# Kernel tuning notes

Hardware: AMD Instinct MI355X
Metric: run time of the kernel (lower is better)

Reference implementation:

```python
import jax, jax.numpy as jnp
import numpy as np

B, L, E = 64, 512, 512       # batch, encoder length, encoder dim
T = 512                      # decoder steps
S, P = 512, 256              # symbols_embedding_dim, prenet_dim
A, D = 1024, 1024            # attention_rnn_dim, decoder_rnn_dim
G, V = 128, 148              # gmm hidden, n_symbols


def setup_inputs() -> dict:
    key = jax.random.key(0)
    ks = jax.random.split(key, 20)
    w = lambda k, shp, s=0.02: (jax.random.normal(k, shp, dtype=jnp.float32) * s)
    memory = jax.random.normal(ks[0], (B, L, E), dtype=jnp.float32)
    decoder_inputs = jax.random.normal(ks[1], (B, S, T), dtype=jnp.float32)
    memory_lengths = jax.random.randint(ks[2], (B,), L // 2, L + 1)
    memory_lengths = memory_lengths.at[0].set(L)  # max length == L (static shapes)
    return {
        'memory': memory,
        'decoder_inputs': decoder_inputs,
        'memory_lengths': memory_lengths,
        'W_pre1': w(ks[3], (S, P)), 'W_pre2': w(ks[4], (P, P)),
        'W_att_ih': w(ks[5], (P + E, 4 * A)), 'W_att_hh': w(ks[6], (A, 4 * A)),
        'b_att_ih': jnp.zeros((4 * A,), jnp.float32), 'b_att_hh': jnp.zeros((4 * A,), jnp.float32),
        'W_g1': w(ks[7], (A, G)), 'b_g1': jnp.zeros((G,), jnp.float32),
        'W_g2': w(ks[8], (G, 2), 0.01),  # original inits this to zero; small random to exercise math
        'W_dec_ih': w(ks[9], (A + E, 4 * D)), 'W_dec_hh': w(ks[10], (D, 4 * D)),
        'b_dec_ih': jnp.zeros((4 * D,), jnp.float32), 'b_dec_hh': jnp.zeros((4 * D,), jnp.float32),
        'W_proj': w(ks[11], (D + E, V)), 'b_proj': jnp.zeros((V,), jnp.float32),
    }


def _lstm_cell(x, h, c, Wih, Whh, bih, bhh):
    # torch.nn.LSTMCell gate order: i, f, g, o
    g = x @ Wih + h @ Whh + bih + bhh
    i, f, gg, o = jnp.split(g, 4, axis=-1)
    c = jax.nn.sigmoid(f) * c + jax.nn.sigmoid(i) * jnp.tanh(gg)
    h = jax.nn.sigmoid(o) * jnp.tanh(c)
    return h, c


def _forward(memory, decoder_inputs, memory_lengths,
             W_pre1, W_pre2, W_att_ih, W_att_hh, b_att_ih, b_att_hh,
             W_g1, b_g1, W_g2, W_dec_ih, W_dec_hh, b_dec_ih, b_dec_hh,
             W_proj, b_proj):
    Bv, Sv, Tv = decoder_inputs.shape
    Lv = memory.shape[1]
    # go frame + teacher-forced inputs: (T+1, B, S)
    x = jnp.concatenate([jnp.zeros((1, Bv, Sv), memory.dtype),
                         jnp.transpose(decoder_inputs, (2, 0, 1))], axis=0)
    # Prenet: dropout is hardcoded training=True in the original
    dk1, dk2 = jax.random.split(jax.random.key(42))
    h1 = jax.nn.relu(x @ W_pre1)
    h1 = h1 * jax.random.bernoulli(dk1, 0.5, h1.shape).astype(h1.dtype) * 2.0
    h2 = jax.nn.relu(h1 @ W_pre2)
    pre = h2 * jax.random.bernoulli(dk2, 0.5, h2.shape).astype(h2.dtype) * 2.0  # (T+1,B,P)

    pad_mask = jnp.arange(Lv)[None, :] >= memory_lengths[:, None]  # (B,L) True on padding
    lin = jnp.arange(Lv, dtype=memory.dtype)[None, :]              # (1,L)

    Av, Dv, Ev = W_att_hh.shape[0], W_dec_hh.shape[0], memory.shape[2]
    init = (jnp.zeros((Bv, Av), memory.dtype), jnp.zeros((Bv, Av), memory.dtype),
            jnp.zeros((Bv, Dv), memory.dtype), jnp.zeros((Bv, Dv), memory.dtype),
            jnp.zeros((Bv, Lv), memory.dtype),  # cumulative attention weights
            jnp.zeros((Bv, Ev), memory.dtype),  # attention context
            jnp.zeros((Bv, 1), memory.dtype))   # GMM mean mu

    def step(carry, x_t):
        ah, ac, dh, dc, cum, ctx, mean = carry
        ah, ac = _lstm_cell(jnp.concatenate([x_t, ctx], -1), ah, ac,
                            W_att_ih, W_att_hh, b_att_ih, b_att_hh)
        # (eval mode: p_attention_dropout inactive)
        h = jnp.tanh(ah @ W_g1 + b_g1) @ W_g2          # (B,2) raw [mean_delta, scale]
        mean = mean + jnp.exp(h[:, :1]) * 8.0
        scale = jnp.exp(h[:, 1:]) * 8.0
        Z = jnp.sqrt(2.0 * np.pi * scale * scale)
        alpha = jnp.exp(-0.5 * (lin - mean) ** 2 / (scale * scale)) / Z  # (B,L)
        alpha = jnp.where(pad_mask, 0.0, alpha)
        ctx = jnp.einsum('bl,ble->be', alpha, memory)
        cum = cum + alpha
        dh, dc = _lstm_cell(jnp.concatenate([ah, ctx], -1), dh, dc,
                            W_dec_ih, W_dec_hh, b_dec_ih, b_dec_hh)
        logit = jnp.concatenate([dh, ctx], -1) @ W_proj + b_proj
        return (ah, ac, dh, dc, cum, ctx, mean), (logit, alpha, h)

    _, (logits, aligns, params) = jax.lax.scan(step, init, pre[:-1])
    return (jnp.transpose(logits, (1, 0, 2)),   # (B,T,V)
            jnp.transpose(aligns, (1, 0, 2)),   # (B,T,L)
            jnp.transpose(params, (1, 0, 2)))   # (B,T,2)


def reference(memory, decoder_inputs, memory_lengths, W_pre1, W_pre2,
              W_att_ih, W_att_hh, b_att_ih, b_att_hh, W_g1, b_g1, W_g2,
              W_dec_ih, W_dec_hh, b_dec_ih, b_dec_hh, W_proj, b_proj):
    return _forward(memory, decoder_inputs, memory_lengths, W_pre1, W_pre2,
                    W_att_ih, W_att_hh, b_att_ih, b_att_hh, W_g1, b_g1, W_g2,
                    W_dec_ih, W_dec_hh, b_dec_ih, b_dec_hh, W_proj, b_proj)
```

## Files before the change

kernel.cpp:

```cpp
#include <hip/hip_runtime.h>
#include <math.h>

#define TF_PARTITIONABLE 1

static constexpr int Bn=64, Ln=512, En=512, Tn=512, Sn=512, Pn=256, An=1024, Dn=1024, Gn=128, Vn=148;
static constexpr int G4A = 4096;
static constexpr int KPROJ = Dn + En;
static constexpr int KATT = 1792, KDEC = 2560;
static constexpr int ACH = 4, ACK = 448;
static constexpr int DCH = 4, DCK = 640;
static constexpr int NKB_ATT = KATT / 32;
static constexpr int NKB_DEC = KDEC / 32;
static constexpr long LOGITS_OFF = 0;
static constexpr long ALIGNS_OFF = (long)Bn*Tn*Vn;
static constexpr long PARAMS_OFF = ALIGNS_OFF + (long)Bn*Tn*Ln;

using s16x8 = __attribute__((ext_vector_type(8))) short;
using f32x4 = __attribute__((ext_vector_type(4))) float;

struct TFo { unsigned a, b; };
static constexpr TFo htf(unsigned k1, unsigned k2, unsigned x0, unsigned x1) {
  unsigned ks2 = k1 ^ k2 ^ 0x1BD11BDAu;
  unsigned ks[3] = {k1, k2, ks2};
  const unsigned ra[4] = {13u,15u,26u,6u}, rb[4] = {17u,29u,16u,24u};
  x0 += k1; x1 += k2;
  for (int g = 0; g < 5; ++g) {
    const unsigned* r = (g % 2 == 0) ? ra : rb;
    for (int i = 0; i < 4; ++i) { x0 += x1; x1 = (x1 << r[i]) | (x1 >> (32u - r[i])); x1 ^= x0; }
    x0 += ks[(g+1)%3]; x1 += ks[(g+2)%3] + (unsigned)(g+1);
  }
  return TFo{x0, x1};
}
#if TF_PARTITIONABLE
static constexpr TFo DK1 = htf(0u,42u,0u,0u);
static constexpr TFo DK2 = htf(0u,42u,0u,1u);
#else
static constexpr TFo S02 = htf(0u,42u,0u,2u);
static constexpr TFo S13 = htf(0u,42u,1u,3u);
static constexpr TFo DK1 = TFo{S02.a, S13.a};
static constexpr TFo DK2 = TFo{S02.b, S13.b};
#endif

__device__ __forceinline__ void dtf(unsigned k1, unsigned k2, unsigned x0, unsigned x1,
                                    unsigned& o0, unsigned& o1) {
  unsigned ks2 = k1 ^ k2 ^ 0x1BD11BDAu;
#define TFR(r) { x0 += x1; x1 = (x1<<r)|(x1>>(32-r)); x1 ^= x0; }
  x0 += k1; x1 += k2;
  TFR(13) TFR(15) TFR(26) TFR(6)  x0 += k2;  x1 += ks2 + 1u;
  TFR(17) TFR(29) TFR(16) TFR(24) x0 += ks2; x1 += k1 + 2u;
  TFR(13) TFR(15) TFR(26) TFR(6)  x0 += k1;  x1 += k2 + 3u;
  TFR(17) TFR(29) TFR(16) TFR(24) x0 += k2;  x1 += ks2 + 4u;
  TFR(13) TFR(15) TFR(26) TFR(6)  x0 += ks2; x1 += k1 + 5u;
#undef TFR
  o0 = x0; o1 = x1;
}

__device__ __forceinline__ bool keepmask(unsigned ka, unsigned kb, unsigned j) {
#if TF_PARTITIONABLE
  unsigned o0, o1; dtf(ka, kb, 0u, j, o0, o1);
  return ((o0 ^ o1) >> 31) == 0u;
#else
  const unsigned H = 4202496u;
  unsigned o0, o1;
  if (j < H) { dtf(ka, kb, j, j + H, o0, o1); return (o0 >> 31) == 0u; }
  else       { dtf(ka, kb, j - H, j, o0, o1); return (o1 >> 31) == 0u; }
#endif
}

__device__ __forceinline__ float ldbf(const unsigned short* p, long i) {
  return __uint_as_float(((unsigned)p[i]) << 16);
}
__device__ __forceinline__ unsigned short f2bf(float v) {
  unsigned x = __float_as_uint(v);
  return (unsigned short)((x + 0x7fffu + ((x >> 16) & 1u)) >> 16);
}
__device__ __forceinline__ void store_out(void* out, long i, float v, int bf) {
  if (bf) ((unsigned short*)out)[i] = f2bf(v);
  else    ((float*)out)[i] = v;
}
__device__ __forceinline__ float st_load(const float* p, long i) { return p[i]; }
__device__ __forceinline__ float st_load(const unsigned short* p, long i) { return ldbf(p, i); }
__device__ __forceinline__ void st_store(float* p, long i, float v) { p[i] = v; }
__device__ __forceinline__ void st_store(unsigned short* p, long i, float v) { p[i] = f2bf(v); }
__device__ __forceinline__ float sigm(float x) { return 1.f / (1.f + expf(-x)); }
__device__ __forceinline__ void st4bf(unsigned short* p, float a, float b, float c, float d) {
  union { unsigned short u[4]; uint2 v; } q;
  q.u[0] = f2bf(a); q.u[1] = f2bf(b); q.u[2] = f2bf(c); q.u[3] = f2bf(d);
  *(uint2*)p = q.v;
}

struct Ptrs {
  const float *Wp1,*Wp2,*bai,*bah,*Wg1,*bg1,*Wg2,*bdi,*bdh,*Wpr,*bpr;
  unsigned short *PWatt,*PWdec,*pre_bf,*ah_bf,*ctx_bf,*dh_bf;
  float *Patt,*Pdec,*ac,*dc,*mean;
  void *dh_all,*ctx_all;
  const void *mem,*din,*w_ai,*w_ah,*w_di,*w_dh;
  const int *mlen; const int *flag; void *out;
};

__global__ __launch_bounds__(256) void k_detect(const void* mem, int* flag) {
  __shared__ int cnt;
  int tid = threadIdx.x;
  if (tid == 0) cnt = 0;
  __syncthreads();
  const unsigned short* p = (const unsigned short*)mem;
  int local = 0;
  for (int i = tid; i < 1024; i += 256) {
    float f = ldbf(p, 2L * i);
    if (f == f && fabsf(f) > 0.0009f && fabsf(f) < 16.f) local++;
  }
  atomicAdd(&cnt, local);
  __syncthreads();
  if (tid == 0) flag[0] = (cnt > 512) ? 1 : 0;
}

__global__ __launch_bounds__(256) void k_convert(const void* src, float* dst, long n, const int* flag) {
  int bf = *flag;
  long i0 = (long)blockIdx.x * 256 + threadIdx.x, stp = (long)gridDim.x * 256;
  if (bf) { const unsigned short* s = (const unsigned short*)src;
            for (long i = i0; i < n; i += stp) dst[i] = ldbf(s, i); }
  else    { const float* s = (const float*)src;
            for (long i = i0; i < n; i += stp) dst[i] = s[i]; }
}

__global__ __launch_bounds__(256) void k_zero_f32(float* p, long n) {
  for (long i = (long)blockIdx.x * 256 + threadIdx.x; i < n; i += (long)gridDim.x * 256) p[i] = 0.f;
}

__global__ __launch_bounds__(256) void k_zero_aligns(void* out, const int* flag) {
  int bf = *flag;
  unsigned* p; long n;
  if (bf) { p = (unsigned*)out + (ALIGNS_OFF >> 1); n = ((long)Bn*Tn*Ln) >> 1; }
  else    { p = (unsigned*)out + ALIGNS_OFF;        n = (long)Bn*Tn*Ln; }
  for (long i = (long)blockIdx.x * 256 + threadIdx.x; i < n; i += (long)gridDim.x * 256) p[i] = 0u;
}

__global__ __launch_bounds__(256) void k_pack(Ptrs P) {
  __shared__ float s[32][65];
  int bid = blockIdx.x, tid = threadIdx.x;
  bool att = bid < NKB_ATT * 64;
  int lb = att ? bid : bid - NKB_ATT * 64;
  int kblk = lb >> 6, ng = lb & 63;
  int n0 = ng * 64;
  int bf = *P.flag;
  int split = att ? (Pn + En) : (An + En);
  const void* S0 = att ? P.w_ai : P.w_di;
  const void* S1 = att ? P.w_ah : P.w_dh;
  for (int i = tid; i < 2048; i += 256) {
    int kk = i >> 6, n = i & 63;
    int k = kblk * 32 + kk;
    const void* src = (k < split) ? S0 : S1;
    long idx = (long)(k < split ? k : k - split) * G4A + (n0 + n);
    s[kk][n] = bf ? ldbf((const unsigned short*)src, idx) : ((const float*)src)[idx];
  }
  __syncthreads();
  int lane = tid & 63, tb = tid >> 6;
  unsigned short r[8];
#pragma unroll
  for (int j = 0; j < 8; ++j)
    r[j] = f2bf(s[(lane >> 4) * 8 + j][tb * 16 + (lane & 15)]);
  unsigned short* out = (att ? P.PWatt : P.PWdec) +
      (((long)kblk * 256 + (ng * 4 + tb)) * 64 + lane) * 8;
  *(uint4*)out = *(const uint4*)r;
}

__global__ __launch_bounds__(256) void k_prenet(Ptrs P, unsigned k1a, unsigned k1b,
                                                unsigned k2a, unsigned k2b) {
  __shared__ __align__(16) float x_s[32 * 17];
  __shared__ __align__(16) float W_s[16 * 256];
  __shared__ __align__(16) float h1_s[32 * 258];
  int bid = blockIdx.x, tid = threadIdx.x;
  int t = bid >> 1, half = bid & 1;
  int bf = *P.flag;
  int tc = tid & 63, tr = tid >> 6;
  int p0 = tc * 4, bl0 = tr * 8;
  float acc[8][4];
#pragma unroll
  for (int i = 0; i < 8; ++i) { acc[i][0]=0; acc[i][1]=0; acc[i][2]=0; acc[i][3]=0; }

  for (int kc = 0; kc < 32; ++kc) {
    __syncthreads();
    for (int i = tid; i < 32 * 16; i += 256) {
      int bl = i >> 4, kk = i & 15;
      int s = kc * 16 + kk;
      float v = 0.f;
      if (t > 0) {
        long idx = ((long)(half * 32 + bl) * Sn + s) * Tn + (t - 1);
        v = bf ? ldbf((const unsigned short*)P.din, idx) : ((const float*)P.din)[idx];
      }
      x_s[bl * 17 + kk] = v;
    }
    for (int i = tid; i < 16 * 256; i += 256) {
      int kk = i >> 8, p = i & 255;
      W_s[kk * 256 + p] = P.Wp1[(long)(kc * 16 + kk) * 256 + p];
    }
    __syncthreads();
    for (int kk = 0; kk < 16; ++kk) {
      float4 w = *(const float4*)(W_s + kk * 256 + p0);
#pragma unroll
      for (int i = 0; i < 8; ++i) {
        float x = x_s[(bl0 + i) * 17 + kk];
        acc[i][0] += x * w.x; acc[i][1] += x * w.y; acc[i][2] += x * w.z; acc[i][3] += x * w.w;
      }
    }
  }
#pragma unroll
  for (int i = 0; i < 8; ++i)
#pragma unroll
    for (int j = 0; j < 4; ++j) {
      int bl = bl0 + i, p = p0 + j, bg = half * 32 + bl;
      float v = fmaxf(acc[i][j], 0.f);
      unsigned ft = (unsigned)(((long)t * 64 + bg) * 256 + p);
      v = keepmask(k1a, k1b, ft) ? 2.f * v : 0.f;
      h1_s[bl * 258 + p] = v;
      acc[i][j] = 0.f;
    }
  __syncthreads();
  for (int kc = 0; kc < 16; ++kc) {
    __syncthreads();
    for (int i = tid; i < 16 * 256; i += 256) {
      int kk = i >> 8, p = i & 255;
      W_s[kk * 256 + p] = P.Wp2[(long)(kc * 16 + kk) * 256 + p];
    }
    __syncthreads();
    for (int kk = 0; kk < 16; ++kk) {
      float4 w = *(const float4*)(W_s + kk * 256 + p0);
      int s = kc * 16 + kk;
#pragma unroll
      for (int i = 0; i < 8; ++i) {
        float x = h1_s[(bl0 + i) * 258 + s];
        acc[i][0] += x * w.x; acc[i][1] += x * w.y; acc[i][2] += x * w.z; acc[i][3] += x * w.w;
      }
    }
  }
#pragma unroll
  for (int i = 0; i < 8; ++i)
#pragma unroll
    for (int j = 0; j < 4; ++j) {
      int bg = half * 32 + bl0 + i, p = p0 + j;
      float v = fmaxf(acc[i][j], 0.f);
      unsigned ft = (unsigned)(((long)t * 64 + bg) * 256 + p);
      v = keepmask(k2a, k2b, ft) ? 2.f * v : 0.f;
      P.pre_bf[((long)t * 64 + bg) * 256 + p] = f2bf(v);
    }
}

template<bool ATT>
__device__ __forceinline__ void dev_gemm(const Ptrs& P, int t, int lb, unsigned short* a_lds) {
  constexpr int CK    = ATT ? ACK : DCK;
  constexpr int SUBK  = CK / 2;
  constexpr int NKS   = SUBK / 32;
  constexpr int PITCH = SUBK + 8;
  constexpr int GPR   = SUBK / 8;
  int tid = threadIdx.x;
  int cg = lb >> 2, kc = lb & 3;
  int lane = tid & 63, w = tid >> 6;
  int nblk = cg * 4 + w;
  const unsigned short* PW = ATT ? P.PWatt : P.PWdec;
  const unsigned short* pre_t = P.pre_bf + (long)(t + 1) * 64 * Pn;
  int rlo = lane & 15, khi8 = (lane >> 4) * 8;

  auto aaddr = [&](int kglob, int row) -> const unsigned short* {
    const unsigned short* seg; int stride; int off;
    if (ATT) {
      if (kglob < Pn)           { seg = pre_t;    stride = Pn; off = kglob; }
      else if (kglob < Pn + En) { seg = P.ctx_bf; stride = En; off = kglob - Pn; }
      else                      { seg = P.ah_bf;  stride = An; off = kglob - Pn - En; }
    } else {
      if (kglob < An)           { seg = P.ah_bf;  stride = An; off = kglob; }
      else if (kglob < An + En) { seg = P.ctx_bf; stride = En; off = kglob - An; }
      else                      { seg = P.dh_bf;  stride = Dn; off = kglob - An - En; }
    }
    return seg + (long)row * stride + off;
  };

  f32x4 acc[4];
#pragma unroll
  for (int i = 0; i < 4; ++i) acc[i] = f32x4{0.f, 0.f, 0.f, 0.f};

#pragma unroll
  for (int sub = 0; sub < 2; ++sub) {
    int k0 = kc * CK + sub * SUBK;
    __syncthreads();
#pragma unroll
    for (int i = 0; i < GPR / 4; ++i) {
      int g = tid + i * 256;
      int row = g / GPR, kg = g - row * GPR;
      *(uint4*)(a_lds + row * PITCH + kg * 8) = *(const uint4*)aaddr(k0 + kg * 8, row);
    }
    __syncthreads();
    const unsigned short* bptr = PW + (((long)(k0 >> 5) * 256 + nblk) * 64 + lane) * 8;
    s16x8 bb0 = *(const s16x8*)bptr;
    s16x8 bb1 = *(const s16x8*)(bptr + 131072);
#pragma unroll
    for (int kb = 0; kb < NKS; ++kb) {
      s16x8 bcur = (kb & 1) ? bb1 : bb0;
      if (kb + 2 < NKS) {
        s16x8 nb = *(const s16x8*)(bptr + (long)(kb + 2) * 131072);
        if (kb & 1) bb1 = nb; else bb0 = nb;
      }
      int abase = kb * 32 + khi8;
#pragma unroll
      for (int mb = 0; mb < 4; ++mb) {
        s16x8 a = *(const s16x8*)(a_lds + (mb * 16 + rlo) * PITCH + abase);
        acc[mb] = __builtin_amdgcn_mfma_f32_16x16x32_bf16(a, bcur, acc[mb], 0, 0, 0);
      }
    }
  }
  float* Pout = (ATT ? P.Patt : P.Pdec) + (long)kc * 64 * G4A;
  int col = nblk * 16 + rlo, rbase = (lane >> 4) * 4;
#pragma unroll
  for (int mb = 0; mb < 4; ++mb)
#pragma unroll
    for (int r = 0; r < 4; ++r)
      Pout[(long)(mb * 16 + rbase + r) * G4A + col] = acc[mb][r];
}

__global__ __launch_bounds__(256) void k_gemm(Ptrs P, int t) {
  __shared__ __align__(16) unsigned short a_lds[64 * 328];
  int bid = blockIdx.x;
  if (bid < 256) { if (t + 1 < Tn) dev_gemm<true>(P, t, bid, a_lds); }
  else           { if (t >= 0 && t < Tn) dev_gemm<false>(P, t, bid - 256, a_lds); }
}

template<typename ST>
__global__ __launch_bounds__(256) void k_point(Ptrs P, int t) {
  __shared__ float ah_s[1024];
  __shared__ float red_s[256];
  __shared__ float tanh_s[128];
  __shared__ float bc_s[2];
  __shared__ float alpha_s[176];
  int bid = blockIdx.x, tid = threadIdx.x;
  if (bid < 64) {
    if (t >= Tn) return;
    int b = bid;
    int bf = *P.flag;
    int u0 = tid * 4;
    float gv[4][4];
#pragma unroll
    for (int gt = 0; gt < 4; ++gt) {
      float4 a = *(const float4*)(P.bai + gt * 1024 + u0);
      float4 c = *(const float4*)(P.bah + gt * 1024 + u0);
      gv[gt][0] = a.x + c.x; gv[gt][1] = a.y + c.y; gv[gt][2] = a.z + c.z; gv[gt][3] = a.w + c.w;
    }
#pragma unroll
    for (int kc = 0; kc < ACH; ++kc) {
      const float* pa = P.Patt + ((long)kc * 64 + b) * G4A + u0;
#pragma unroll
      for (int gt = 0; gt < 4; ++gt) {
        float4 v = *(const float4*)(pa + gt * 1024);
        gv[gt][0] += v.x; gv[gt][1] += v.y; gv[gt][2] += v.z; gv[gt][3] += v.w;
      }
    }
    float4 oc = *(const float4*)(P.ac + b * 1024 + u0);
    float oldc[4] = {oc.x, oc.y, oc.z, oc.w};
    float hh[4], cc[4];
#pragma unroll
    for (int i = 0; i < 4; ++i) {
      float ii = sigm(gv[0][i]), ff = sigm(gv[1][i]), oo = sigm(gv[3][i]);
      cc[i] = ff * oldc[i] + ii * tanhf(gv[2][i]);
      hh[i] = oo * tanhf(cc[i]);
      ah_s[u0 + i] = hh[i];
    }
    *(float4*)(P.ac + b * 1024 + u0) = make_float4(cc[0], cc[1], cc[2], cc[3]);
    st4bf(P.ah_bf + b * 1024 + u0, hh[0], hh[1], hh[2], hh[3]);
    __syncthreads();
    {
      int g = tid & 127, hf = tid >> 7;
      const float* wg = P.Wg1 + g;
      float a0 = 0.f, a1 = 0.f;
      int ub = hf * 512;
      for (int u = ub; u < ub + 512; u += 2) {
        a0 += ah_s[u]     * wg[(long)u * 128];
        a1 += ah_s[u + 1] * wg[(long)(u + 1) * 128];
      }
      red_s[tid] = a0 + a1;
    }
    __syncthreads();
    if (tid < 128) tanh_s[tid] = tanhf(red_s[tid] + red_s[tid + 128] + P.bg1[tid]);
    __syncthreads();
    if (tid < 64) {
      float tv0 = tanh_s[tid], tv1 = tanh_s[tid + 64];
      float h0 = tv0 * P.Wg2[2 * tid]     + tv1 * P.Wg2[2 * (tid + 64)];
      float h1 = tv0 * P.Wg2[2 * tid + 1] + tv1 * P.Wg2[2 * (tid + 64) + 1];
#pragma unroll
      for (int o = 32; o; o >>= 1) { h0 += __shfl_down(h0, o); h1 += __shfl_down(h1, o); }
      if (tid == 0) {
        float m  = P.mean[b] + expf(h0) * 8.f;
        float sc = expf(h1) * 8.f;
        P.mean[b] = m;
        long pidx = PARAMS_OFF + ((long)b * Tn + t) * 2;
        store_out(P.out, pidx, h0, bf);
        store_out(P.out, pidx + 1, h1, bf);
        bc_s[0] = m; bc_s[1] = sc;
      }
    }
    __syncthreads();
    float m = bc_s[0], sc = bc_s[1];
    int len = P.mlen[b];
    int ci = (int)floorf(fminf(m, 100000.f));
    int l0 = ci - 80; if (l0 < 0) l0 = 0;
    int l1 = ci + 81; if (l1 > len) l1 = len;
    float inv2 = 0.5f / (sc * sc);
    float invZ = 1.f / (2.50662827463100050242f * sc);
    for (int l = l0 + tid; l < l1; l += 256) {
      float d = (float)l - m;
      float al = expf(-d * d * inv2) * invZ;
      alpha_s[l - l0] = al;
      store_out(P.out, ALIGNS_OFF + ((long)b * Tn + t) * Ln + l, al, bf);
    }
    __syncthreads();
    int nl = l1 - l0;
    ST* ctx_all = (ST*)P.ctx_all;
    int e0 = tid * 2;
    float s0 = 0.f, s1 = 0.f;
    if (bf) {
      const unsigned short* mem = (const unsigned short*)P.mem + ((long)b * Ln + l0) * En + e0;
      for (int l = 0; l < nl; ++l) {
        float al = alpha_s[l];
        s0 += al * ldbf(mem, (long)l * En);
        s1 += al * ldbf(mem, (long)l * En + 1);
      }
    } else {
      const float* mem = (const float*)P.mem + ((long)b * Ln + l0) * En + e0;
      for (int l = 0; l < nl; ++l) {
        float al = alpha_s[l];
        s0 += al * mem[(long)l * En];
        s1 += al * mem[(long)l * En + 1];
      }
    }
    unsigned q = (unsigned)f2bf(s0) | ((unsigned)f2bf(s1) << 16);
    *(unsigned*)(P.ctx_bf + b * En + e0) = q;
    st_store(ctx_all, ((long)t * 64 + b) * En + e0, s0);
    st_store(ctx_all, ((long)t * 64 + b) * En + e0 + 1, s1);
  } else {
    if (t == 0) return;
    int bb = bid - 64;
    int b = bb * 2 + (tid >> 7);
    int u0 = (tid & 127) * 8;
    ST* dh_all = (ST*)P.dh_all;
    float gv[4][8];
#pragma unroll
    for (int gt = 0; gt < 4; ++gt) {
      float4 a0 = *(const float4*)(P.bdi + gt * 1024 + u0);
      float4 a1 = *(const float4*)(P.bdi + gt * 1024 + u0 + 4);
      float4 c0 = *(const float4*)(P.bdh + gt * 1024 + u0);
      float4 c1 = *(const float4*)(P.bdh + gt * 1024 + u0 + 4);
      gv[gt][0] = a0.x + c0.x; gv[gt][1] = a0.y + c0.y; gv[gt][2] = a0.z + c0.z; gv[gt][3] = a0.w + c0.w;
      gv[gt][4] = a1.x + c1.x; gv[gt][5] = a1.y + c1.y; gv[gt][6] = a1.z + c1.z; gv[gt][7] = a1.w + c1.w;
    }
#pragma unroll
    for (int kc = 0; kc < DCH; ++kc) {
      const float* pd = P.Pdec + ((long)kc * 64 + b) * G4A + u0;
#pragma unroll
      for (int gt = 0; gt < 4; ++gt) {
        float4 v0 = *(const float4*)(pd + gt * 1024);
        float4 v1 = *(const float4*)(pd + gt * 1024 + 4);
        gv[gt][0] += v0.x; gv[gt][1] += v0.y; gv[gt][2] += v0.z; gv[gt][3] += v0.w;
        gv[gt][4] += v1.x; gv[gt][5] += v1.y; gv[gt][6] += v1.z; gv[gt][7] += v1.w;
      }
    }
    float4 oc0 = *(const float4*)(P.dc + b * 1024 + u0);
    float4 oc1 = *(const float4*)(P.dc + b * 1024 + u0 + 4);
    float oldc[8] = {oc0.x, oc0.y, oc0.z, oc0.w, oc1.x, oc1.y, oc1.z, oc1.w};
    float hh[8], cc[8];
#pragma unroll
    for (int i = 0; i < 8; ++i) {
      float ii = sigm(gv[0][i]), ff = sigm(gv[1][i]), oo = sigm(gv[3][i]);
      cc[i] = ff * oldc[i] + ii * tanhf(gv[2][i]);
      hh[i] = oo * tanhf(cc[i]);
    }
    *(float4*)(P.dc + b * 1024 + u0)     = make_float4(cc[0], cc[1], cc[2], cc[3]);
    *(float4*)(P.dc + b * 1024 + u0 + 4) = make_float4(cc[4], cc[5], cc[6], cc[7]);
    st4bf(P.dh_bf + b * 1024 + u0,     hh[0], hh[1], hh[2], hh[3]);
    st4bf(P.dh_bf + b * 1024 + u0 + 4, hh[4], hh[5], hh[6], hh[7]);
#pragma unroll
    for (int i = 0; i < 8; ++i)
      st_store(dh_all, ((long)(t - 1) * 64 + b) * 1024 + u0 + i, hh[i]);
  }
}

template<typename ST>
__global__ __launch_bounds__(256) void k_proj(Ptrs P) {
  __shared__ __align__(16) float A_s[64][65];
  __shared__ __align__(16) float W_s[64 * 160];
  int t = blockIdx.x, tid = threadIdx.x;
  int bf = *P.flag;
  const ST* dh_all = (const ST*)P.dh_all;
  const ST* ctx_all = (const ST*)P.ctx_all;
  int tc = tid & 15, tr = tid >> 4;
  int c0 = tc * 10, b0 = tr * 4;
  float acc[4][10];
#pragma unroll
  for (int i = 0; i < 4; ++i)
#pragma unroll
    for (int j = 0; j < 10; ++j) acc[i][j] = 0.f;
  for (int k0 = 0; k0 < KPROJ; k0 += 64) {
    __syncthreads();
    for (int i = tid; i < 64 * 64; i += 256) {
      int b = i >> 6, kk = i & 63;
      int k = k0 + kk;
      float v = (k < Dn) ? st_load(dh_all, ((long)t * 64 + b) * Dn + k)
                         : st_load(ctx_all, ((long)t * 64 + b) * En + (k - Dn));
      A_s[b][kk] = v;
    }
    for (int i = tid; i < 64 * 160; i += 256) {
      int kk = i / 160, c = i - kk * 160;
      W_s[kk * 160 + c] = (c < Vn) ? P.Wpr[(long)(k0 + kk) * Vn + c] : 0.f;
    }
    __syncthreads();
    for (int kk = 0; kk < 64; ++kk) {
      float xs[4];
#pragma unroll
      for (int i = 0; i < 4; ++i) xs[i] = A_s[b0 + i][kk];
#pragma unroll
      for (int j = 0; j < 10; ++j) {
        float w = W_s[kk * 160 + c0 + j];
#pragma unroll
        for (int i = 0; i < 4; ++i) acc[i][j] += xs[i] * w;
      }
    }
  }
#pragma unroll
  for (int i = 0; i < 4; ++i)
#pragma unroll
    for (int j = 0; j < 10; ++j) {
      int c = c0 + j;
      if (c < Vn) {
        int b = b0 + i;
        store_out(P.out, LOGITS_OFF + ((long)b * Tn + t) * Vn + c, acc[i][j] + P.bpr[c], bf);
      }
    }
}

template<typename ST>
static void run_pipeline(const Ptrs& P, hipStream_t stream) {
  k_prenet<<<Tn * 2, 256, 0, stream>>>(P, DK1.a, DK1.b, DK2.a, DK2.b);
  k_gemm<<<512, 256, 0, stream>>>(P, -1);
  for (int t = 0; t <= Tn; ++t) {
    k_point<ST><<<96, 256, 0, stream>>>(P, t);
    if (t < Tn) k_gemm<<<512, 256, 0, stream>>>(P, t);
  }
  k_proj<ST><<<Tn, 256, 0, stream>>>(P);
}

extern "C" void kernel_launch(void* const* d_in, const int* in_sizes, int n_in,
                              void* d_out, int out_size, void* d_ws, size_t ws_size,
                              hipStream_t stream) {
  (void)in_sizes; (void)n_in; (void)out_size;
  char* base = (char*)d_ws;
  int* flag = (int*)base;
  size_t off = 256;
  auto allocf = [&](size_t n) -> float* {
    float* p = (float*)(base + off);
    off += ((n * 4 + 255) / 256) * 256;
    return p;
  };
  auto allocu = [&](size_t n) -> unsigned short* {
    unsigned short* p = (unsigned short*)(base + off);
    off += ((n * 2 + 255) / 256) * 256;
    return p;
  };
  float* Wp1 = allocf(131072);
  float* Wp2 = allocf(65536);
  float* bai = allocf(4096);
  float* bah = allocf(4096);
  float* Wg1 = allocf(131072);
  float* bg1 = allocf(128);
  float* Wg2 = allocf(256);
  float* bdi = allocf(4096);
  float* bdh = allocf(4096);
  float* Wpr = allocf(227328);
  float* bpr = allocf(148);
  unsigned short* PWatt = allocu((size_t)NKB_ATT * 256 * 512);
  unsigned short* PWdec = allocu((size_t)NKB_DEC * 256 * 512);
  unsigned short* pre_bf = allocu((size_t)Tn * 64 * Pn);
  float* Patt = allocf((size_t)ACH * 64 * G4A);
  float* Pdec = allocf((size_t)DCH * 64 * G4A);
  float* ac = allocf(65536);
  float* dc = allocf(65536);
  float* mean = allocf(64);
  unsigned short* ah_bf = allocu(65536);
  unsigned short* ctx_bf = allocu(32768);
  unsigned short* dh_bf = allocu(65536);
  size_t fixed = off;
  size_t nDH = (size_t)Tn * 64 * Dn, nCX = (size_t)Tn * 64 * En;
  bool f32tier = (fixed + (nDH + nCX) * 4 <= ws_size);
  bool b16tier = (fixed + (nDH + nCX) * 2 <= ws_size);
  if (!f32tier && !b16tier) return;

  Ptrs P;
  P.Wp1=Wp1; P.Wp2=Wp2; P.bai=bai; P.bah=bah; P.Wg1=Wg1; P.bg1=bg1; P.Wg2=Wg2;
  P.bdi=bdi; P.bdh=bdh; P.Wpr=Wpr; P.bpr=bpr;
  P.PWatt=PWatt; P.PWdec=PWdec; P.pre_bf=pre_bf;
  P.ah_bf=ah_bf; P.ctx_bf=ctx_bf; P.dh_bf=dh_bf;
  P.Patt=Patt; P.Pdec=Pdec; P.ac=ac; P.dc=dc; P.mean=mean;
  size_t esz = f32tier ? 4 : 2;
  P.dh_all  = base + fixed;
  P.ctx_all = base + fixed + nDH * esz;
  P.mem = d_in[0]; P.din = d_in[1]; P.mlen = (const int*)d_in[2];
  P.w_ai = d_in[5]; P.w_ah = d_in[6]; P.w_di = d_in[12]; P.w_dh = d_in[13];
  P.flag = flag; P.out = d_out;

  k_detect<<<1, 256, 0, stream>>>(d_in[0], flag);

  struct CV { const void* s; float* d; long n; };
  const CV cv[11] = {
    {d_in[3], Wp1, 131072}, {d_in[4], Wp2, 65536},
    {d_in[7], bai, 4096}, {d_in[8], bah, 4096},
    {d_in[9], Wg1, 131072}, {d_in[10], bg1, 128}, {d_in[11], Wg2, 256},
    {d_in[14], bdi, 4096}, {d_in[15], bdh, 4096},
    {d_in[16], Wpr, 227328}, {d_in[17], bpr, 148},
  };
  for (int i = 0; i < 11; ++i) {
    long g = (cv[i].n + 255) / 256; if (g > 1024) g = 1024;
    k_convert<<<(int)g, 256, 0, stream>>>(cv[i].s, cv[i].d, cv[i].n, flag);
  }
  k_pack<<<(NKB_ATT + NKB_DEC) * 64, 256, 0, stream>>>(P);
  k_zero_f32<<<512, 256, 0, stream>>>(ac, 131136 + 81920);
  k_zero_aligns<<<2048, 256, 0, stream>>>(d_out, flag);

  if (f32tier) run_pipeline<float>(P, stream);
  else         run_pipeline<unsigned short>(P, stream);
}
```

Before: 17.32 ms.

## Pack GEMM A operands into contiguous per-step buffers and pipeline loads

Replaces the per-segment A-operand address lambda with two contiguous bf16 activation buffers (attA, decA) that the pointwise kernel writes into directly, so the step GEMM loads a single strided matrix. The GEMM now prefetches the second K half into registers while the first half runs and deepens B prefetch to four buffers. The pointwise kernel is relaunched with 1024-thread blocks handling four (or eight) batch rows each to cut block count. This adds duplicate stores of ah/ctx into both buffers and more register pressure in the GEMM.

```diff
diff --git a/kernel.cpp b/kernel.cpp
--- a/kernel.cpp
+++ b/kernel.cpp
@@ -88,10 +88,16 @@
   q.u[0] = f2bf(a); q.u[1] = f2bf(b); q.u[2] = f2bf(c); q.u[3] = f2bf(d);
   *(uint2*)p = q.v;
 }
+__device__ __forceinline__ void st8bf(unsigned short* p, const float* h) {
+  union { unsigned short u[8]; uint4 v; } q;
+#pragma unroll
+  for (int i = 0; i < 8; ++i) q.u[i] = f2bf(h[i]);
+  *(uint4*)p = q.v;
+}
 
 struct Ptrs {
   const float *Wp1,*Wp2,*bai,*bah,*Wg1,*bg1,*Wg2,*bdi,*bdh,*Wpr,*bpr;
-  unsigned short *PWatt,*PWdec,*pre_bf,*ah_bf,*ctx_bf,*dh_bf;
+  unsigned short *PWatt,*PWdec,*pre_bf,*attA,*decA;
   float *Patt,*Pdec,*ac,*dc,*mean;
   void *dh_all,*ctx_all;
   const void *mem,*din,*w_ai,*w_ah,*w_di,*w_dh;
@@ -133,6 +139,15 @@
   if (bf) { p = (unsigned*)out + (ALIGNS_OFF >> 1); n = ((long)Bn*Tn*Ln) >> 1; }
   else    { p = (unsigned*)out + ALIGNS_OFF;        n = (long)Bn*Tn*Ln; }
   for (long i = (long)blockIdx.x * 256 + threadIdx.x; i < n; i += (long)gridDim.x * 256) p[i] = 0u;
+}
+
+__global__ __launch_bounds__(256) void k_precopy(Ptrs P) {
+  int tid = threadIdx.x;
+  for (int i = tid; i < 2048; i += 256) {
+    int b = i >> 5, g = i & 31;
+    *(uint4*)(P.attA + (long)b * KATT + g * 8) =
+        *(const uint4*)(P.pre_bf + (long)b * Pn + g * 8);
+  }
 }
 
 __global__ __launch_bounds__(256) void k_pack(Ptrs P) {
@@ -246,59 +261,54 @@
 }
 
 template<bool ATT>
-__device__ __forceinline__ void dev_gemm(const Ptrs& P, int t, int lb, unsigned short* a_lds) {
+__device__ __forceinline__ void dev_gemm(const Ptrs& P, int lb, unsigned short* a_lds) {
   constexpr int CK    = ATT ? ACK : DCK;
   constexpr int SUBK  = CK / 2;
   constexpr int NKS   = SUBK / 32;
   constexpr int PITCH = SUBK + 8;
   constexpr int GPR   = SUBK / 8;
+  constexpr int NLD   = GPR / 4;
+  constexpr int KSTR  = ATT ? KATT : KDEC;
   int tid = threadIdx.x;
   int cg = lb >> 2, kc = lb & 3;
   int lane = tid & 63, w = tid >> 6;
   int nblk = cg * 4 + w;
   const unsigned short* PW = ATT ? P.PWatt : P.PWdec;
-  const unsigned short* pre_t = P.pre_bf + (long)(t + 1) * 64 * Pn;
+  const unsigned short* A  = ATT ? P.attA : P.decA;
   int rlo = lane & 15, khi8 = (lane >> 4) * 8;
-
-  auto aaddr = [&](int kglob, int row) -> const unsigned short* {
-    const unsigned short* seg; int stride; int off;
-    if (ATT) {
-      if (kglob < Pn)           { seg = pre_t;    stride = Pn; off = kglob; }
-      else if (kglob < Pn + En) { seg = P.ctx_bf; stride = En; off = kglob - Pn; }
-      else                      { seg = P.ah_bf;  stride = An; off = kglob - Pn - En; }
-    } else {
-      if (kglob < An)           { seg = P.ah_bf;  stride = An; off = kglob; }
-      else if (kglob < An + En) { seg = P.ctx_bf; stride = En; off = kglob - An; }
-      else                      { seg = P.dh_bf;  stride = Dn; off = kglob - An - En; }
-    }
-    return seg + (long)row * stride + off;
-  };
+  const int k0 = kc * CK;
+
+  int srow[NLD], scol[NLD];
+#pragma unroll
+  for (int i = 0; i < NLD; ++i) {
+    int g = tid + i * 256;
+    srow[i] = g / GPR; scol[i] = (g - srow[i] * GPR) * 8;
+  }
+  uint4 areg[NLD];
+#pragma unroll
+  for (int i = 0; i < NLD; ++i)
+    areg[i] = *(const uint4*)(A + (long)srow[i] * KSTR + k0 + scol[i]);
+#pragma unroll
+  for (int i = 0; i < NLD; ++i)
+    *(uint4*)(a_lds + srow[i] * PITCH + scol[i]) = areg[i];
+  __syncthreads();
+#pragma unroll
+  for (int i = 0; i < NLD; ++i)
+    areg[i] = *(const uint4*)(A + (long)srow[i] * KSTR + k0 + SUBK + scol[i]);
 
   f32x4 acc[4];
 #pragma unroll
   for (int i = 0; i < 4; ++i) acc[i] = f32x4{0.f, 0.f, 0.f, 0.f};
 
-#pragma unroll
-  for (int sub = 0; sub < 2; ++sub) {
-    int k0 = kc * CK + sub * SUBK;
-    __syncthreads();
-#pragma unroll
-    for (int i = 0; i < GPR / 4; ++i) {
-      int g = tid + i * 256;
-      int row = g / GPR, kg = g - row * GPR;
-      *(uint4*)(a_lds + row * PITCH + kg * 8) = *(const uint4*)aaddr(k0 + kg * 8, row);
-    }
-    __syncthreads();
+  {
     const unsigned short* bptr = PW + (((long)(k0 >> 5) * 256 + nblk) * 64 + lane) * 8;
-    s16x8 bb0 = *(const s16x8*)bptr;
-    s16x8 bb1 = *(const s16x8*)(bptr + 131072);
+    s16x8 br[4];
+#pragma unroll
+    for (int i = 0; i < 4; ++i) if (i < NKS) br[i] = *(const s16x8*)(bptr + (long)i * 131072);
 #pragma unroll
     for (int kb = 0; kb < NKS; ++kb) {
-      s16x8 bcur = (kb & 1) ? bb1 : bb0;
-      if (kb + 2 < NKS) {
-        s16x8 nb = *(const s16x8*)(bptr + (long)(kb + 2) * 131072);
-        if (kb & 1) bb1 = nb; else bb0 = nb;
-      }
+      s16x8 bcur = br[kb & 3];
+      if (kb + 4 < NKS) br[kb & 3] = *(const s16x8*)(bptr + (long)(kb + 4) * 131072);
       int abase = kb * 32 + khi8;
 #pragma unroll
       for (int mb = 0; mb < 4; ++mb) {
@@ -307,6 +317,28 @@
       }
     }
   }
+  __syncthreads();
+#pragma unroll
+  for (int i = 0; i < NLD; ++i)
+    *(uint4*)(a_lds + srow[i] * PITCH + scol[i]) = areg[i];
+  __syncthreads();
+  {
+    const unsigned short* bptr = PW + (((long)((k0 + SUBK) >> 5) * 256 + nblk) * 64 + lane) * 8;
+    s16x8 br[4];
+#pragma unroll
+    for (int i = 0; i < 4; ++i) if (i < NKS) br[i] = *(const s16x8*)(bptr + (long)i * 131072);
+#pragma unroll
+    for (int kb = 0; kb < NKS; ++kb) {
+      s16x8 bcur = br[kb & 3];
+      if (kb + 4 < NKS) br[kb & 3] = *(const s16x8*)(bptr + (long)(kb + 4) * 131072);
+      int abase = kb * 32 + khi8;
+#pragma unroll
+      for (int mb = 0; mb < 4; ++mb) {
+        s16x8 a = *(const s16x8*)(a_lds + (mb * 16 + rlo) * PITCH + abase);
+        acc[mb] = __builtin_amdgcn_mfma_f32_16x16x32_bf16(a, bcur, acc[mb], 0, 0, 0);
+      }
+    }
+  }
   float* Pout = (ATT ? P.Patt : P.Pdec) + (long)kc * 64 * G4A;
   int col = nblk * 16 + rlo, rbase = (lane >> 4) * 4;
 #pragma unroll
@@ -319,23 +351,33 @@
 __global__ __launch_bounds__(256) void k_gemm(Ptrs P, int t) {
   __shared__ __align__(16) unsigned short a_lds[64 * 328];
   int bid = blockIdx.x;
-  if (bid < 256) { if (t + 1 < Tn) dev_gemm<true>(P, t, bid, a_lds); }
-  else           { if (t >= 0 && t < Tn) dev_gemm<false>(P, t, bid - 256, a_lds); }
+  if (bid < 256) { if (t + 1 < Tn) dev_gemm<true>(P, bid, a_lds); }
+  else           { if (t >= 0 && t < Tn) dev_gemm<false>(P, bid - 256, a_lds); }
 }
 
 template<typename ST>
-__global__ __launch_bounds__(256) void k_point(Ptrs P, int t) {
-  __shared__ float ah_s[1024];
-  __shared__ float red_s[256];
-  __shared__ float tanh_s[128];
-  __shared__ float bc_s[2];
-  __shared__ float alpha_s[176];
+__global__ __launch_bounds__(1024) void k_point(Ptrs P, int t) {
+  __shared__ float ah_sh[4 * 1024];
+  __shared__ float red_sh[4 * 256];
+  __shared__ float tanh_sh[4 * 128];
+  __shared__ float bc_sh[4 * 2];
+  __shared__ float al_sh[4 * 176];
   int bid = blockIdx.x, tid = threadIdx.x;
-  if (bid < 64) {
+  if (bid < 16) {
     if (t >= Tn) return;
-    int b = bid;
+    int h = tid >> 8, ltid = tid & 255;
+    int b = bid * 4 + h;
+    float* ah_s = ah_sh + h * 1024;
+    float* red_s = red_sh + h * 256;
+    float* tanh_s = tanh_sh + h * 128;
+    float* bc_s = bc_sh + h * 2;
+    float* alpha_s = al_sh + h * 176;
     int bf = *P.flag;
-    int u0 = tid * 4;
+    if (t + 1 < Tn && ltid < 32) {
+      *(uint4*)(P.attA + (long)b * KATT + ltid * 8) =
+          *(const uint4*)(P.pre_bf + ((long)(t + 1) * 64 + b) * Pn + ltid * 8);
+    }
+    int u0 = ltid * 4;
     float gv[4][4];
 #pragma unroll
     for (int gt = 0; gt < 4; ++gt) {
@@ -363,10 +405,11 @@
       ah_s[u0 + i] = hh[i];
     }
     *(float4*)(P.ac + b * 1024 + u0) = make_float4(cc[0], cc[1], cc[2], cc[3]);
-    st4bf(P.ah_bf + b * 1024 + u0, hh[0], hh[1], hh[2], hh[3]);
+    st4bf(P.attA + (long)b * KATT + 768 + u0, hh[0], hh[1], hh[2], hh[3]);
+    st4bf(P.decA + (long)b * KDEC + u0,       hh[0], hh[1], hh[2], hh[3]);
     __syncthreads();
     {
-      int g = tid & 127, hf = tid >> 7;
+      int g = ltid & 127, hf = ltid >> 7;
       const float* wg = P.Wg1 + g;
       float a0 = 0.f, a1 = 0.f;
       int ub = hf * 512;
@@ -374,18 +417,18 @@
         a0 += ah_s[u]     * wg[(long)u * 128];
         a1 += ah_s[u + 1] * wg[(long)(u + 1) * 128];
       }
-      red_s[tid] = a0 + a1;
-    }
-    __syncthreads();
-    if (tid < 128) tanh_s[tid] = tanhf(red_s[tid] + red_s[tid + 128] + P.bg1[tid]);
-    __syncthreads();
-    if (tid < 64) {
-      float tv0 = tanh_s[tid], tv1 = tanh_s[tid + 64];
-      float h0 = tv0 * P.Wg2[2 * tid]     + tv1 * P.Wg2[2 * (tid + 64)];
-      float h1 = tv0 * P.Wg2[2 * tid + 1] + tv1 * P.Wg2[2 * (tid + 64) + 1];
+      red_s[ltid] = a0 + a1;
+    }
+    __syncthreads();
+    if (ltid < 128) tanh_s[ltid] = tanhf(red_s[ltid] + red_s[ltid + 128] + P.bg1[ltid]);
+    __syncthreads();
+    if (ltid < 64) {
+      float tv0 = tanh_s[ltid], tv1 = tanh_s[ltid + 64];
+      float h0 = tv0 * P.Wg2[2 * ltid]     + tv1 * P.Wg2[2 * (ltid + 64)];
+      float h1 = tv0 * P.Wg2[2 * ltid + 1] + tv1 * P.Wg2[2 * (ltid + 64) + 1];
 #pragma unroll
       for (int o = 32; o; o >>= 1) { h0 += __shfl_down(h0, o); h1 += __shfl_down(h1, o); }
-      if (tid == 0) {
+      if (ltid == 0) {
         float m  = P.mean[b] + expf(h0) * 8.f;
         float sc = expf(h1) * 8.f;
         P.mean[b] = m;
@@ -403,7 +446,7 @@
     int l1 = ci + 81; if (l1 > len) l1 = len;
     float inv2 = 0.5f / (sc * sc);
     float invZ = 1.f / (2.50662827463100050242f * sc);
-    for (int l = l0 + tid; l < l1; l += 256) {
+    for (int l = l0 + ltid; l < l1; l += 256) {
       float d = (float)l - m;
       float al = expf(-d * d * inv2) * invZ;
       alpha_s[l - l0] = al;
@@ -412,7 +455,7 @@
     __syncthreads();
     int nl = l1 - l0;
     ST* ctx_all = (ST*)P.ctx_all;
-    int e0 = tid * 2;
+    int e0 = ltid * 2;
     float s0 = 0.f, s1 = 0.f;
     if (bf) {
       const unsigned short* mem = (const unsigned short*)P.mem + ((long)b * Ln + l0) * En + e0;
@@ -430,13 +473,14 @@
       }
     }
     unsigned q = (unsigned)f2bf(s0) | ((unsigned)f2bf(s1) << 16);
-    *(unsigned*)(P.ctx_bf + b * En + e0) = q;
+    *(unsigned*)(P.attA + (long)b * KATT + 256 + e0) = q;
+    *(unsigned*)(P.decA + (long)b * KDEC + 1024 + e0) = q;
     st_store(ctx_all, ((long)t * 64 + b) * En + e0, s0);
     st_store(ctx_all, ((long)t * 64 + b) * En + e0 + 1, s1);
   } else {
     if (t == 0) return;
-    int bb = bid - 64;
-    int b = bb * 2 + (tid >> 7);
+    int bb = bid - 16;
+    int b = bb * 8 + (tid >> 7);
     int u0 = (tid & 127) * 8;
     ST* dh_all = (ST*)P.dh_all;
     float gv[4][8];
@@ -472,8 +516,7 @@
     }
     *(float4*)(P.dc + b * 1024 + u0)     = make_float4(cc[0], cc[1], cc[2], cc[3]);
     *(float4*)(P.dc + b * 1024 + u0 + 4) = make_float4(cc[4], cc[5], cc[6], cc[7]);
-    st4bf(P.dh_bf + b * 1024 + u0,     hh[0], hh[1], hh[2], hh[3]);
-    st4bf(P.dh_bf + b * 1024 + u0 + 4, hh[4], hh[5], hh[6], hh[7]);
+    st8bf(P.decA + (long)b * KDEC + 1536 + u0, hh);
 #pragma unroll
     for (int i = 0; i < 8; ++i)
       st_store(dh_all, ((long)(t - 1) * 64 + b) * 1024 + u0 + i, hh[i]);
@@ -536,9 +579,10 @@
 template<typename ST>
 static void run_pipeline(const Ptrs& P, hipStream_t stream) {
   k_prenet<<<Tn * 2, 256, 0, stream>>>(P, DK1.a, DK1.b, DK2.a, DK2.b);
+  k_precopy<<<1, 256, 0, stream>>>(P);
   k_gemm<<<512, 256, 0, stream>>>(P, -1);
   for (int t = 0; t <= Tn; ++t) {
-    k_point<ST><<<96, 256, 0, stream>>>(P, t);
+    k_point<ST><<<24, 1024, 0, stream>>>(P, t);
     if (t < Tn) k_gemm<<<512, 256, 0, stream>>>(P, t);
   }
   k_proj<ST><<<Tn, 256, 0, stream>>>(P);
@@ -580,9 +624,8 @@
   float* ac = allocf(65536);
   float* dc = allocf(65536);
   float* mean = allocf(64);
-  unsigned short* ah_bf = allocu(65536);
-  unsigned short* ctx_bf = allocu(32768);
-  unsigned short* dh_bf = allocu(65536);
+  unsigned short* attA = allocu((size_t)64 * KATT);
+  unsigned short* decA = allocu((size_t)64 * KDEC);
   size_t fixed = off;
   size_t nDH = (size_t)Tn * 64 * Dn, nCX = (size_t)Tn * 64 * En;
   bool f32tier = (fixed + (nDH + nCX) * 4 <= ws_size);
@@ -592,8 +635,7 @@
   Ptrs P;
   P.Wp1=Wp1; P.Wp2=Wp2; P.bai=bai; P.bah=bah; P.Wg1=Wg1; P.bg1=bg1; P.Wg2=Wg2;
   P.bdi=bdi; P.bdh=bdh; P.Wpr=Wpr; P.bpr=bpr;
-  P.PWatt=PWatt; P.PWdec=PWdec; P.pre_bf=pre_bf;
-  P.ah_bf=ah_bf; P.ctx_bf=ctx_bf; P.dh_bf=dh_bf;
+  P.PWatt=PWatt; P.PWdec=PWdec; P.pre_bf=pre_bf; P.attA=attA; P.decA=decA;
   P.Patt=Patt; P.Pdec=Pdec; P.ac=ac; P.dc=dc; P.mean=mean;
   size_t esz = f32tier ? 4 : 2;
   P.dh_all  = base + fixed;
@@ -617,7 +659,7 @@
     k_convert<<<(int)g, 256, 0, stream>>>(cv[i].s, cv[i].d, cv[i].n, flag);
   }
   k_pack<<<(NKB_ATT + NKB_DEC) * 64, 256, 0, stream>>>(P);
-  k_zero_f32<<<512, 256, 0, stream>>>(ac, 131136 + 81920);
+  k_zero_f32<<<512, 256, 0, stream>>>(ac, 131136 + 57344 + 81920);
   k_zero_aligns<<<2048, 256, 0, stream>>>(d_out, flag);
 
   if (f32tier) run_pipeline<float>(P, stream);
```

New measurement: 31.08 ms. +79.4%, slower.
